# Performance work log

Hardware: AMD Instinct MI355X
Metric: run time of the kernel (lower is better)

## Reference

```python
import jax, jax.numpy as jnp
import numpy as np

B, D, T, R = 8, 128, 32768, 2
C = D // R  # reduced channel dim = 64


def conv1x1(x, w, b):
    # x: [B, Cin, T], w: [Cout, Cin], b: [Cout] -> [B, Cout, T]
    return jnp.einsum('oi,bit->bot', w, x) + b[None, :, None]


def setup_inputs() -> dict:
    key = jax.random.key(0)
    ks = jax.random.split(key, 16)
    inp = {
        'x1': jax.random.normal(ks[0], (B, D, T), dtype=jnp.float32),
        'x2': jnp.zeros((B, D, T), dtype=jnp.float32),  # unused in encoder stage
        'mask': jnp.ones((B, 1, T), dtype=jnp.float32),
        # 1x1 conv projections (weights squeezed to [out, in])
        'wq': jax.random.normal(ks[1], (C, D), dtype=jnp.float32) * 0.05,
        'bq': jnp.zeros((C,), dtype=jnp.float32),
        'wk': jax.random.normal(ks[2], (C, D), dtype=jnp.float32) * 0.05,
        'bk': jnp.zeros((C,), dtype=jnp.float32),
        'wv': jax.random.normal(ks[3], (C, D), dtype=jnp.float32) * 0.05,
        'bv': jnp.zeros((C,), dtype=jnp.float32),
        # E, F: Linear(C -> C) with bias
        'we': jax.random.normal(ks[4], (C, C), dtype=jnp.float32) * 0.1,
        'be': jnp.zeros((C,), dtype=jnp.float32),
        'wf': jax.random.normal(ks[5], (C, C), dtype=jnp.float32) * 0.1,
        'bf': jnp.zeros((C,), dtype=jnp.float32),
        # output 1x1 conv: C -> D
        'wo': jax.random.normal(ks[6], (D, C), dtype=jnp.float32) * 0.05,
        'bo': jnp.zeros((D,), dtype=jnp.float32),
    }
    return inp


def reference(x1, x2, mask, wq, bq, wk, bk, wv, bv, we, be, wf, bf, wo, bo):
    # Q/K/V projections (encoder stage: value from x1; x2 unused)
    Q = conv1x1(x1, wq, bq)              # [B, C, T]
    K = conv1x1(x1, wk, bk)              # [B, C, T]
    V = conv1x1(x1, wv, bv)              # [B, C, T]
    # K = E(K^T): [B, T, C] @ we^T + be
    Kp = jnp.einsum('bct,oc->bto', K, we) + be  # [B, T, C]
    # S = Q @ Kp -> [B, C, C], scaled by sqrt(last dim)
    S = jnp.einsum('bct,btk->bck', Q, Kp)
    P = jax.nn.softmax(S / jnp.sqrt(jnp.asarray(S.shape[-1], S.dtype)), axis=-1)
    # dropout is identity in eval mode
    # V = (F(V^T))^T: [B, C, T]
    Vp = jnp.einsum('bct,oc->bot', V, wf) + bf[None, :, None]  # [B, C, T]
    out = jnp.einsum('bck,bkt->bct', P, Vp)  # [B, C, T]
    out = conv1x1(jax.nn.relu(out), wo, bo)  # [B, D, T]
    return out * mask[:, 0:1, :]
```

## Files before the change

### kernel.cpp

```cpp
#include <hip/hip_runtime.h>
#include <stdint.h>
#include <stddef.h>

#define B_ 8
#define D_ 128
#define T_ 32768
#define C_ 64
#define NCH_ 128

typedef __bf16 bf16;
typedef __bf16 bf16x4 __attribute__((ext_vector_type(4)));
typedef __bf16 bf16x8 __attribute__((ext_vector_type(8)));
typedef float f32x4 __attribute__((ext_vector_type(4)));
typedef float f32x16 __attribute__((ext_vector_type(16)));

__device__ __forceinline__ f32x16 zero16() {
  f32x16 z;
#pragma unroll
  for (int i = 0; i < 16; ++i) z[i] = 0.f;
  return z;
}

__global__ __launch_bounds__(256) void k0_zero(float* __restrict__ p, int n)
{
  int i = blockIdx.x * 256 + threadIdx.x;
  if (i < n) p[i] = 0.f;
}

__global__ __launch_bounds__(256, 4) void k1_gram(
    const float* __restrict__ x1,
    const float* __restrict__ we, const float* __restrict__ wk,
    const float* __restrict__ bk, const float* __restrict__ be,
    const float* __restrict__ wf, const float* __restrict__ wv,
    const float* __restrict__ bv, const float* __restrict__ bfv,
    const float* __restrict__ wo,
    float* __restrict__ G, float* __restrict__ r,
    float* __restrict__ wkp, float* __restrict__ wvp,
    float* __restrict__ bkp, float* __restrict__ bvp,
    bf16* __restrict__ wobf,
    float* __restrict__ gpart)
{
  const int blk = blockIdx.x;
  const int tid = threadIdx.x;
  const int ngram = B_ * NCH_;

  if (blk >= ngram) {
    const int wb = blk - ngram;
    if (wb < 64) {
      const float* wa  = (wb < 32) ? we : wf;
      const float* wb2 = (wb < 32) ? wk : wv;
      float* outw      = (wb < 32) ? wkp : wvp;
      const int idx = (wb & 31) * 256 + tid;
      const int o = idx >> 7, d = idx & 127;
      float s = 0.f;
      for (int c = 0; c < 64; ++c) s += wa[o * 64 + c] * wb2[c * 128 + d];
      outw[idx] = s;
      if (tid < 64) {
        if (wb == 0) {
          float t = 0.f;
          for (int c = 0; c < 64; ++c) t += we[tid * 64 + c] * bk[c];
          bkp[tid] = t + be[tid];
        } else if (wb == 32) {
          float t = 0.f;
          for (int c = 0; c < 64; ++c) t += wf[tid * 64 + c] * bv[c];
          bvp[tid] = t + bfv[tid];
        }
      }
    } else {
      const int idx = (wb - 64) * 256 + tid;
      wobf[idx] = (bf16)wo[idx];
    }
    return;
  }

  __shared__ bf16 x_s[128 * 72];

  const int b  = blk >> 7;
  const int ch = blk & (NCH_ - 1);
  const int t0 = ch * (T_ / NCH_);
  const int wave = tid >> 6, lane = tid & 63;
  const int lrow = lane & 31, lk = lane >> 5;
  const int qa = wave >> 1, qb = wave & 1;

  const float* xb = x1 + (size_t)b * D_ * T_;

  f32x16 acc00 = zero16(), acc01 = zero16(), acc10 = zero16(), acc11 = zero16();
  float rsum = 0.f;

  const int scol = (tid & 15) * 4;
  const int srow0 = tid >> 4;

  const bf16* A0  = &x_s[(64 * qa + lrow) * 72 + 8 * lk];
  const bf16* A1  = A0 + 32 * 72;
  const bf16* Bb0 = &x_s[(64 * qb + lrow) * 72 + 8 * lk];
  const bf16* Bb1 = Bb0 + 32 * 72;

  f32x4 pre[8];
#pragma unroll
  for (int it = 0; it < 8; ++it) {
    const int row = it * 16 + srow0;
    pre[it] = *(const f32x4*)(xb + (size_t)row * T_ + t0 + scol);
  }

  for (int s = 0; s < 4; ++s) {
    if (s) __syncthreads();
#pragma unroll
    for (int it = 0; it < 8; ++it) {
      const int row = it * 16 + srow0;
      bf16x4 h;
#pragma unroll
      for (int j = 0; j < 4; ++j) h[j] = (bf16)pre[it][j];
      *(bf16x4*)&x_s[row * 72 + scol] = h;
    }
    __syncthreads();
    if (s < 3) {
      const int tb = t0 + (s + 1) * 64;
#pragma unroll
      for (int it = 0; it < 8; ++it) {
        const int row = it * 16 + srow0;
        pre[it] = *(const f32x4*)(xb + (size_t)row * T_ + tb + scol);
      }
    }
#pragma unroll
    for (int k = 0; k < 4; ++k) {
      bf16x8 fa0 = *(const bf16x8*)(A0 + 16 * k);
      bf16x8 fa1 = *(const bf16x8*)(A1 + 16 * k);
      bf16x8 fb0 = *(const bf16x8*)(Bb0 + 16 * k);
      bf16x8 fb1 = *(const bf16x8*)(Bb1 + 16 * k);
      bf16x8 own = qb ? fa1 : fa0;
#pragma unroll
      for (int j = 0; j < 8; ++j) rsum += (float)own[j];
      acc00 = __builtin_amdgcn_mfma_f32_32x32x16_bf16(fa0, fb0, acc00, 0, 0, 0);
      acc01 = __builtin_amdgcn_mfma_f32_32x32x16_bf16(fa0, fb1, acc01, 0, 0, 0);
      acc10 = __builtin_amdgcn_mfma_f32_32x32x16_bf16(fa1, fb0, acc10, 0, 0, 0);
      acc11 = __builtin_amdgcn_mfma_f32_32x32x16_bf16(fa1, fb1, acc11, 0, 0, 0);
    }
  }

  if (gpart) {
    float* gp = gpart + (size_t)blk * 16384;
#pragma unroll
    for (int rr = 0; rr < 16; ++rr) {
      const int rloc = (rr & 3) + 8 * (rr >> 2) + 4 * lk;
      const int r0 = 64 * qa + rloc, r1 = 64 * qa + 32 + rloc;
      const int c0 = 64 * qb + lrow, c1 = 64 * qb + 32 + lrow;
      gp[r0 * 128 + c0] = acc00[rr];
      gp[r0 * 128 + c1] = acc01[rr];
      gp[r1 * 128 + c0] = acc10[rr];
      gp[r1 * 128 + c1] = acc11[rr];
    }
  } else {
    float* gb = G + (size_t)b * 16384;
#pragma unroll
    for (int rr = 0; rr < 16; ++rr) {
      const int rloc = (rr & 3) + 8 * (rr >> 2) + 4 * lk;
      const int r0 = 64 * qa + rloc, r1 = 64 * qa + 32 + rloc;
      const int c0 = 64 * qb + lrow, c1 = 64 * qb + 32 + lrow;
      atomicAdd(&gb[r0 * 128 + c0], acc00[rr]);
      atomicAdd(&gb[r0 * 128 + c1], acc01[rr]);
      atomicAdd(&gb[r1 * 128 + c0], acc10[rr]);
      atomicAdd(&gb[r1 * 128 + c1], acc11[rr]);
    }
  }
  float rtot = rsum + __shfl_xor(rsum, 32, 64);
  if (lk == 0) atomicAdd(&r[b * 128 + 32 * wave + lrow], rtot);
}

__global__ __launch_bounds__(256) void k2_reduce(
    const float* __restrict__ gpart, float* __restrict__ G)
{
  const int g4 = blockIdx.x * 256 + threadIdx.x;
  const int b = g4 >> 12;
  const int e4 = g4 & 4095;
  const f32x4* p = (const f32x4*)(gpart + ((size_t)b * NCH_) * 16384) + e4;
  f32x4 s = {0.f, 0.f, 0.f, 0.f};
#pragma unroll 8
  for (int ch = 0; ch < NCH_; ++ch) s += p[(size_t)ch * 4096];
  *((f32x4*)G + g4) = s;
}

__global__ __launch_bounds__(128) void k3_softmax(
    const float* __restrict__ wq, const float* __restrict__ bq,
    const float* __restrict__ G, const float* __restrict__ r,
    const float* __restrict__ wkp, const float* __restrict__ wvp,
    const float* __restrict__ bkp, const float* __restrict__ bvp,
    bf16* __restrict__ attw, float* __restrict__ attb)
{
  const int b = blockIdx.x >> 6, c = blockIdx.x & 63;
  const int tid = threadIdx.x;
  __shared__ float sM[128], sR[128], sQ[128], sP[64];
  __shared__ float sRed;

  const float* Gb = G + (size_t)b * 16384;
  const float* wqc = wq + c * 128;

  const float rv = r[b * 128 + tid];
  sR[tid] = rv;
  float m = 0.f;
  for (int j = 0; j < 128; ++j) m += wqc[j] * Gb[j * 128 + tid];
  sM[tid] = m;
  sQ[tid] = wqc[tid] * rv;
  __syncthreads();

  if (tid < 64) {
    float q2 = sQ[tid] + sQ[tid + 64];
#pragma unroll
    for (int off = 32; off; off >>= 1) q2 += __shfl_xor(q2, off, 64);
    if (tid == 0) sRed = q2;
  }
  __syncthreads();
  const float qr = sRed;
  const float bqc = bq[c];

  if (tid < 64) {
    const int k = tid;
    float s = 0.f, wkr = 0.f;
    for (int i = 0; i < 128; ++i) {
      const float w = wkp[k * 128 + i];
      s += sM[i] * w;
      wkr += sR[i] * w;
    }
    const float bk2 = bkp[k];
    float logit = (s + bqc * wkr + bk2 * qr + (float)T_ * bqc * bk2) * 0.125f;
    float mx = logit;
#pragma unroll
    for (int off = 32; off; off >>= 1) mx = fmaxf(mx, __shfl_xor(mx, off, 64));
    const float e = __expf(logit - mx);
    float sum = e;
#pragma unroll
    for (int off = 32; off; off >>= 1) sum += __shfl_xor(sum, off, 64);
    sP[k] = e / sum;
  }
  __syncthreads();

  {
    float aw = 0.f;
    for (int k = 0; k < 64; ++k) aw += sP[k] * wvp[k * 128 + tid];
    attw[((size_t)b * 64 + c) * 128 + tid] = (bf16)aw;
  }
  if (tid < 64) {
    float pb = sP[tid] * bvp[tid];
#pragma unroll
    for (int off = 32; off; off >>= 1) pb += __shfl_xor(pb, off, 64);
    if (tid == 0) attb[b * 64 + c] = pb;
  }
}

__global__ __launch_bounds__(256, 4) void k4_out(
    const float* __restrict__ x1, const float* __restrict__ mask,
    const bf16* __restrict__ wobf, const float* __restrict__ bo,
    const bf16* __restrict__ attw, const float* __restrict__ attb,
    float* __restrict__ out)
{
  __shared__ bf16 m1[128 * 72];
  __shared__ float bo_s[128];
  __shared__ float ab_s[64];

  const int b = blockIdx.x >> 8;
  const int t0 = (blockIdx.x & 255) << 7;
  const int tid = threadIdx.x;
  const int wave = tid >> 6, lane = tid & 63;
  const int lrow = lane & 31, lk = lane >> 5;
  const int tcol = 32 * wave + lrow;

  if (tid < 128) bo_s[tid] = bo[tid];
  if (tid < 64) ab_s[tid] = attb[b * 64 + tid];
  __syncthreads();

  const float* xc = x1 + (size_t)b * D_ * T_ + t0 + tcol;
  const bf16* awb = attw + (size_t)b * 8192;

  f32x16 p0 = zero16(), p1 = zero16();
#pragma unroll
  for (int k0 = 0; k0 < 8; ++k0) {
    bf16x8 a0 = *(const bf16x8*)(awb + (size_t)lrow * 128 + 16 * k0 + 8 * lk);
    bf16x8 a1 = *(const bf16x8*)(awb + (size_t)(32 + lrow) * 128 + 16 * k0 + 8 * lk);
    bf16x8 bx;
#pragma unroll
    for (int j = 0; j < 8; ++j)
      bx[j] = (bf16)xc[(size_t)(16 * k0 + 8 * lk + j) * T_];
    p0 = __builtin_amdgcn_mfma_f32_32x32x16_bf16(a0, bx, p0, 0, 0, 0);
    p1 = __builtin_amdgcn_mfma_f32_32x32x16_bf16(a1, bx, p1, 0, 0, 0);
  }
  bf16* mrow = &m1[tcol * 72];
#pragma unroll
  for (int rr = 0; rr < 16; ++rr) {
    const int row = (rr & 3) + 8 * (rr >> 2) + 4 * lk;
    mrow[row]      = (bf16)fmaxf(p0[rr] + ab_s[row], 0.f);
    mrow[32 + row] = (bf16)fmaxf(p1[rr] + ab_s[32 + row], 0.f);
  }

  f32x16 q0 = zero16(), q1 = zero16(), q2 = zero16(), q3 = zero16();
#pragma unroll
  for (int k0 = 0; k0 < 4; ++k0) {
    bf16x8 bm = *(const bf16x8*)(mrow + 16 * k0 + 8 * lk);
    bf16x8 w0 = *(const bf16x8*)(wobf + (size_t)(lrow) * 64 + 16 * k0 + 8 * lk);
    bf16x8 w1 = *(const bf16x8*)(wobf + (size_t)(32 + lrow) * 64 + 16 * k0 + 8 * lk);
    bf16x8 w2 = *(const bf16x8*)(wobf + (size_t)(64 + lrow) * 64 + 16 * k0 + 8 * lk);
    bf16x8 w3 = *(const bf16x8*)(wobf + (size_t)(96 + lrow) * 64 + 16 * k0 + 8 * lk);
    q0 = __builtin_amdgcn_mfma_f32_32x32x16_bf16(w0, bm, q0, 0, 0, 0);
    q1 = __builtin_amdgcn_mfma_f32_32x32x16_bf16(w1, bm, q1, 0, 0, 0);
    q2 = __builtin_amdgcn_mfma_f32_32x32x16_bf16(w2, bm, q2, 0, 0, 0);
    q3 = __builtin_amdgcn_mfma_f32_32x32x16_bf16(w3, bm, q3, 0, 0, 0);
  }

  const float mv = mask[(size_t)b * T_ + t0 + tcol];
  float* ob = out + (size_t)b * D_ * T_ + t0 + tcol;
#pragma unroll
  for (int rr = 0; rr < 16; ++rr) {
    const int row = (rr & 3) + 8 * (rr >> 2) + 4 * lk;
    ob[(size_t)(row) * T_]      = (q0[rr] + bo_s[row]) * mv;
    ob[(size_t)(32 + row) * T_] = (q1[rr] + bo_s[32 + row]) * mv;
    ob[(size_t)(64 + row) * T_] = (q2[rr] + bo_s[64 + row]) * mv;
    ob[(size_t)(96 + row) * T_] = (q3[rr] + bo_s[96 + row]) * mv;
  }
}

extern "C" void kernel_launch(void* const* d_in, const int* in_sizes, int n_in,
                              void* d_out, int out_size, void* d_ws, size_t ws_size,
                              hipStream_t stream)
{
  const float* x1   = (const float*)d_in[0];
  const float* mask = (const float*)d_in[2];
  const float* wq   = (const float*)d_in[3];
  const float* bq   = (const float*)d_in[4];
  const float* wk   = (const float*)d_in[5];
  const float* bk   = (const float*)d_in[6];
  const float* wv   = (const float*)d_in[7];
  const float* bv   = (const float*)d_in[8];
  const float* we   = (const float*)d_in[9];
  const float* be   = (const float*)d_in[10];
  const float* wf   = (const float*)d_in[11];
  const float* bfv  = (const float*)d_in[12];
  const float* wo   = (const float*)d_in[13];
  const float* bo   = (const float*)d_in[14];
  float* out = (float*)d_out;

  char* base = (char*)d_ws;
  size_t off = 0;
  float* G    = (float*)(base + off); off += (size_t)B_ * 16384 * 4;
  float* r    = (float*)(base + off); off += (size_t)B_ * 128 * 4;
  float* wkp  = (float*)(base + off); off += 8192 * 4;
  float* wvp  = (float*)(base + off); off += 8192 * 4;
  float* bkp  = (float*)(base + off); off += 64 * 4;
  float* bvp  = (float*)(base + off); off += 64 * 4;
  float* attb = (float*)(base + off); off += (size_t)B_ * 64 * 4;
  bf16* attw  = (bf16*)(base + off);  off += (size_t)B_ * 64 * 128 * 2;
  bf16* wobf  = (bf16*)(base + off);  off += 8192 * 2;
  off = (off + 15) & ~(size_t)15;
  float* gpart = (float*)(base + off);
  const size_t need = off + (size_t)B_ * NCH_ * 16384 * 4;
  const bool use_part = (ws_size >= need);
  if (!use_part) gpart = nullptr;

  if (use_part) {
    k0_zero<<<(B_ * 128 + 255) / 256, 256, 0, stream>>>(r, B_ * 128);
  } else {
    const int nzero = B_ * 16384 + B_ * 128;
    k0_zero<<<(nzero + 255) / 256, 256, 0, stream>>>(G, nzero);
  }
  k1_gram<<<B_ * NCH_ + 96, 256, 0, stream>>>(
      x1, we, wk, bk, be, wf, wv, bv, bfv, wo,
      G, r, wkp, wvp, bkp, bvp, wobf, gpart);
  if (use_part)
    k2_reduce<<<(B_ * 16384) / (256 * 4), 256, 0, stream>>>(gpart, G);
  k3_softmax<<<B_ * 64, 128, 0, stream>>>(wq, bq, G, r, wkp, wvp, bkp, bvp, attw, attb);
  k4_out<<<B_ * (T_ / 128), 256, 0, stream>>>(x1, mask, wobf, bo, attw, attb, out);
}
```

Before: 435.6 us.

## Stage x and output through LDS for coalesced loads and stores in gram and output kernels

The gram kernel now loads the whole 256-column chunk into LDS in one pass instead of four double-buffered 64-column stages. Partial gram tiles are written as contiguous per-wave vectors, and the reduce kernel scatters them into the final layout. The output kernel replaces strided per-element x loads with coalesced row loads transposed into LDS. It also stages results through LDS so global stores become row-contiguous. Occupancy hints drop from 4 to 2 blocks to accommodate the larger shared memory, which costs latency hiding.

```diff
diff --git a/kernel.cpp b/kernel.cpp
--- a/kernel.cpp
+++ b/kernel.cpp
@@ -11,6 +11,7 @@
 typedef __bf16 bf16;
 typedef __bf16 bf16x4 __attribute__((ext_vector_type(4)));
 typedef __bf16 bf16x8 __attribute__((ext_vector_type(8)));
+typedef float f32x2 __attribute__((ext_vector_type(2)));
 typedef float f32x4 __attribute__((ext_vector_type(4)));
 typedef float f32x16 __attribute__((ext_vector_type(16)));
 
@@ -27,7 +28,7 @@
   if (i < n) p[i] = 0.f;
 }
 
-__global__ __launch_bounds__(256, 4) void k1_gram(
+__global__ __launch_bounds__(256, 2) void k1_gram(
     const float* __restrict__ x1,
     const float* __restrict__ we, const float* __restrict__ wk,
     const float* __restrict__ bk, const float* __restrict__ be,
@@ -73,7 +74,7 @@
     return;
   }
 
-  __shared__ bf16 x_s[128 * 72];
+  __shared__ bf16 x_s[128 * 264];
 
   const int b  = blk >> 7;
   const int ch = blk & (NCH_ - 1);
@@ -82,72 +83,57 @@
   const int lrow = lane & 31, lk = lane >> 5;
   const int qa = wave >> 1, qb = wave & 1;
 
-  const float* xb = x1 + (size_t)b * D_ * T_;
+  const float* xb = x1 + (size_t)b * D_ * T_ + t0;
+
+#pragma unroll
+  for (int g = 0; g < 4; ++g) {
+    f32x4 pre[8];
+#pragma unroll
+    for (int i = 0; i < 8; ++i) {
+      const int row = 32 * wave + 8 * g + i;
+      pre[i] = *(const f32x4*)(xb + (size_t)row * T_ + 4 * lane);
+    }
+#pragma unroll
+    for (int i = 0; i < 8; ++i) {
+      const int row = 32 * wave + 8 * g + i;
+      bf16x4 h;
+#pragma unroll
+      for (int j = 0; j < 4; ++j) h[j] = (bf16)pre[i][j];
+      *(bf16x4*)&x_s[row * 264 + 4 * lane] = h;
+    }
+  }
+  __syncthreads();
 
   f32x16 acc00 = zero16(), acc01 = zero16(), acc10 = zero16(), acc11 = zero16();
   float rsum = 0.f;
 
-  const int scol = (tid & 15) * 4;
-  const int srow0 = tid >> 4;
-
-  const bf16* A0  = &x_s[(64 * qa + lrow) * 72 + 8 * lk];
-  const bf16* A1  = A0 + 32 * 72;
-  const bf16* Bb0 = &x_s[(64 * qb + lrow) * 72 + 8 * lk];
-  const bf16* Bb1 = Bb0 + 32 * 72;
-
-  f32x4 pre[8];
-#pragma unroll
-  for (int it = 0; it < 8; ++it) {
-    const int row = it * 16 + srow0;
-    pre[it] = *(const f32x4*)(xb + (size_t)row * T_ + t0 + scol);
-  }
-
-  for (int s = 0; s < 4; ++s) {
-    if (s) __syncthreads();
-#pragma unroll
-    for (int it = 0; it < 8; ++it) {
-      const int row = it * 16 + srow0;
-      bf16x4 h;
-#pragma unroll
-      for (int j = 0; j < 4; ++j) h[j] = (bf16)pre[it][j];
-      *(bf16x4*)&x_s[row * 72 + scol] = h;
-    }
-    __syncthreads();
-    if (s < 3) {
-      const int tb = t0 + (s + 1) * 64;
-#pragma unroll
-      for (int it = 0; it < 8; ++it) {
-        const int row = it * 16 + srow0;
-        pre[it] = *(const f32x4*)(xb + (size_t)row * T_ + tb + scol);
-      }
-    }
-#pragma unroll
-    for (int k = 0; k < 4; ++k) {
-      bf16x8 fa0 = *(const bf16x8*)(A0 + 16 * k);
-      bf16x8 fa1 = *(const bf16x8*)(A1 + 16 * k);
-      bf16x8 fb0 = *(const bf16x8*)(Bb0 + 16 * k);
-      bf16x8 fb1 = *(const bf16x8*)(Bb1 + 16 * k);
-      bf16x8 own = qb ? fa1 : fa0;
-#pragma unroll
-      for (int j = 0; j < 8; ++j) rsum += (float)own[j];
-      acc00 = __builtin_amdgcn_mfma_f32_32x32x16_bf16(fa0, fb0, acc00, 0, 0, 0);
-      acc01 = __builtin_amdgcn_mfma_f32_32x32x16_bf16(fa0, fb1, acc01, 0, 0, 0);
-      acc10 = __builtin_amdgcn_mfma_f32_32x32x16_bf16(fa1, fb0, acc10, 0, 0, 0);
-      acc11 = __builtin_amdgcn_mfma_f32_32x32x16_bf16(fa1, fb1, acc11, 0, 0, 0);
-    }
+  const bf16* A0  = &x_s[(64 * qa + lrow) * 264 + 8 * lk];
+  const bf16* A1  = A0 + 32 * 264;
+  const bf16* Bb0 = &x_s[(64 * qb + lrow) * 264 + 8 * lk];
+  const bf16* Bb1 = Bb0 + 32 * 264;
+
+#pragma unroll
+  for (int k = 0; k < 16; ++k) {
+    bf16x8 fa0 = *(const bf16x8*)(A0 + 16 * k);
+    bf16x8 fa1 = *(const bf16x8*)(A1 + 16 * k);
+    bf16x8 fb0 = *(const bf16x8*)(Bb0 + 16 * k);
+    bf16x8 fb1 = *(const bf16x8*)(Bb1 + 16 * k);
+    bf16x8 own = qb ? fa1 : fa0;
+#pragma unroll
+    for (int j = 0; j < 8; ++j) rsum += (float)own[j];
+    acc00 = __builtin_amdgcn_mfma_f32_32x32x16_bf16(fa0, fb0, acc00, 0, 0, 0);
+    acc01 = __builtin_amdgcn_mfma_f32_32x32x16_bf16(fa0, fb1, acc01, 0, 0, 0);
+    acc10 = __builtin_amdgcn_mfma_f32_32x32x16_bf16(fa1, fb0, acc10, 0, 0, 0);
+    acc11 = __builtin_amdgcn_mfma_f32_32x32x16_bf16(fa1, fb1, acc11, 0, 0, 0);
   }
 
   if (gpart) {
-    float* gp = gpart + (size_t)blk * 16384;
+    float* gp = gpart + (size_t)blk * 16384 + wave * 4096;
 #pragma unroll
     for (int rr = 0; rr < 16; ++rr) {
-      const int rloc = (rr & 3) + 8 * (rr >> 2) + 4 * lk;
-      const int r0 = 64 * qa + rloc, r1 = 64 * qa + 32 + rloc;
-      const int c0 = 64 * qb + lrow, c1 = 64 * qb + 32 + lrow;
-      gp[r0 * 128 + c0] = acc00[rr];
-      gp[r0 * 128 + c1] = acc01[rr];
-      gp[r1 * 128 + c0] = acc10[rr];
-      gp[r1 * 128 + c1] = acc11[rr];
+      f32x4 v;
+      v[0] = acc00[rr]; v[1] = acc01[rr]; v[2] = acc10[rr]; v[3] = acc11[rr];
+      *(f32x4*)(gp + rr * 256 + lane * 4) = v;
     }
   } else {
     float* gb = G + (size_t)b * 16384;
@@ -176,7 +162,17 @@
   f32x4 s = {0.f, 0.f, 0.f, 0.f};
 #pragma unroll 8
   for (int ch = 0; ch < NCH_; ++ch) s += p[(size_t)ch * 4096];
-  *((f32x4*)G + g4) = s;
+
+  const int w = e4 >> 10, rr = (e4 >> 6) & 15, lane = e4 & 63;
+  const int lk = lane >> 5, lrow = lane & 31;
+  const int qa = w >> 1, qb = w & 1;
+  const int rloc = (rr & 3) + 8 * (rr >> 2) + 4 * lk;
+  const int r0 = 64 * qa + rloc, c0 = 64 * qb + lrow;
+  float* Gb = G + (size_t)b * 16384;
+  Gb[r0 * 128 + c0]               = s[0];
+  Gb[r0 * 128 + c0 + 32]          = s[1];
+  Gb[(r0 + 32) * 128 + c0]        = s[2];
+  Gb[(r0 + 32) * 128 + c0 + 32]   = s[3];
 }
 
 __global__ __launch_bounds__(128) void k3_softmax(
@@ -246,13 +242,16 @@
   }
 }
 
-__global__ __launch_bounds__(256, 4) void k4_out(
+__global__ __launch_bounds__(256, 2) void k4_out(
     const float* __restrict__ x1, const float* __restrict__ mask,
     const bf16* __restrict__ wobf, const float* __restrict__ bo,
     const bf16* __restrict__ attw, const float* __restrict__ attb,
     float* __restrict__ out)
 {
-  __shared__ bf16 m1[128 * 72];
+  __shared__ __attribute__((aligned(16))) char buf[128 * 136 * 2];
+  bf16*  x_st = (bf16*)buf;
+  float* o_s  = (float*)buf;
+  __shared__ bf16 m1t[128 * 72];
   __shared__ float bo_s[128];
   __shared__ float ab_s[64];
 
@@ -261,36 +260,49 @@
   const int tid = threadIdx.x;
   const int wave = tid >> 6, lane = tid & 63;
   const int lrow = lane & 31, lk = lane >> 5;
-  const int tcol = 32 * wave + lrow;
 
   if (tid < 128) bo_s[tid] = bo[tid];
   if (tid < 64) ab_s[tid] = attb[b * 64 + tid];
-  __syncthreads();
-
-  const float* xc = x1 + (size_t)b * D_ * T_ + t0 + tcol;
+
+  const float* xb = x1 + (size_t)b * D_ * T_ + t0;
+#pragma unroll
+  for (int g = 0; g < 4; ++g) {
+    f32x2 pr[8];
+#pragma unroll
+    for (int i = 0; i < 8; ++i) {
+      const int d = 32 * wave + 8 * g + i;
+      pr[i] = *(const f32x2*)(xb + (size_t)d * T_ + 2 * lane);
+    }
+#pragma unroll
+    for (int i = 0; i < 8; ++i) {
+      const int d = 32 * wave + 8 * g + i;
+      x_st[(2 * lane) * 136 + d]     = (bf16)pr[i][0];
+      x_st[(2 * lane + 1) * 136 + d] = (bf16)pr[i][1];
+    }
+  }
+  __syncthreads();
+
   const bf16* awb = attw + (size_t)b * 8192;
-
-  f32x16 p0 = zero16(), p1 = zero16();
-#pragma unroll
-  for (int k0 = 0; k0 < 8; ++k0) {
-    bf16x8 a0 = *(const bf16x8*)(awb + (size_t)lrow * 128 + 16 * k0 + 8 * lk);
-    bf16x8 a1 = *(const bf16x8*)(awb + (size_t)(32 + lrow) * 128 + 16 * k0 + 8 * lk);
-    bf16x8 bx;
-#pragma unroll
-    for (int j = 0; j < 8; ++j)
-      bx[j] = (bf16)xc[(size_t)(16 * k0 + 8 * lk + j) * T_];
-    p0 = __builtin_amdgcn_mfma_f32_32x32x16_bf16(a0, bx, p0, 0, 0, 0);
-    p1 = __builtin_amdgcn_mfma_f32_32x32x16_bf16(a1, bx, p1, 0, 0, 0);
-  }
-  bf16* mrow = &m1[tcol * 72];
+  f32x16 m0 = zero16(), m1a = zero16();
+  const bf16* ax = &x_st[(32 * wave + lrow) * 136 + 8 * lk];
+#pragma unroll
+  for (int ki = 0; ki < 8; ++ki) {
+    bf16x8 af = *(const bf16x8*)(ax + 16 * ki);
+    bf16x8 b0 = *(const bf16x8*)(awb + (size_t)lrow * 128 + 16 * ki + 8 * lk);
+    bf16x8 b1 = *(const bf16x8*)(awb + (size_t)(32 + lrow) * 128 + 16 * ki + 8 * lk);
+    m0  = __builtin_amdgcn_mfma_f32_32x32x16_bf16(af, b0, m0, 0, 0, 0);
+    m1a = __builtin_amdgcn_mfma_f32_32x32x16_bf16(af, b1, m1a, 0, 0, 0);
+  }
 #pragma unroll
   for (int rr = 0; rr < 16; ++rr) {
-    const int row = (rr & 3) + 8 * (rr >> 2) + 4 * lk;
-    mrow[row]      = (bf16)fmaxf(p0[rr] + ab_s[row], 0.f);
-    mrow[32 + row] = (bf16)fmaxf(p1[rr] + ab_s[32 + row], 0.f);
-  }
+    const int tl = 32 * wave + (rr & 3) + 8 * (rr >> 2) + 4 * lk;
+    m1t[tl * 72 + lrow]      = (bf16)fmaxf(m0[rr]  + ab_s[lrow], 0.f);
+    m1t[tl * 72 + 32 + lrow] = (bf16)fmaxf(m1a[rr] + ab_s[32 + lrow], 0.f);
+  }
+  __syncthreads();
 
   f32x16 q0 = zero16(), q1 = zero16(), q2 = zero16(), q3 = zero16();
+  const bf16* mrow = &m1t[(32 * wave + lrow) * 72];
 #pragma unroll
   for (int k0 = 0; k0 < 4; ++k0) {
     bf16x8 bm = *(const bf16x8*)(mrow + 16 * k0 + 8 * lk);
@@ -304,15 +316,37 @@
     q3 = __builtin_amdgcn_mfma_f32_32x32x16_bf16(w3, bm, q3, 0, 0, 0);
   }
 
-  const float mv = mask[(size_t)b * T_ + t0 + tcol];
-  float* ob = out + (size_t)b * D_ * T_ + t0 + tcol;
+  const int tl = 32 * wave + lrow;
+  const float mv = mask[(size_t)b * T_ + t0 + tl];
+  float* ob = out + (size_t)b * D_ * T_ + t0;
+
 #pragma unroll
   for (int rr = 0; rr < 16; ++rr) {
-    const int row = (rr & 3) + 8 * (rr >> 2) + 4 * lk;
-    ob[(size_t)(row) * T_]      = (q0[rr] + bo_s[row]) * mv;
-    ob[(size_t)(32 + row) * T_] = (q1[rr] + bo_s[32 + row]) * mv;
-    ob[(size_t)(64 + row) * T_] = (q2[rr] + bo_s[64 + row]) * mv;
-    ob[(size_t)(96 + row) * T_] = (q3[rr] + bo_s[96 + row]) * mv;
+    const int rloc = (rr & 3) + 8 * (rr >> 2) + 4 * lk;
+    o_s[rloc * 132 + tl]        = (q0[rr] + bo_s[rloc]) * mv;
+    o_s[(32 + rloc) * 132 + tl] = (q1[rr] + bo_s[32 + rloc]) * mv;
+  }
+  __syncthreads();
+#pragma unroll
+  for (int i = 0; i < 16; ++i) {
+    const int dl = 16 * wave + i;
+    f32x2 v = *(const f32x2*)(o_s + dl * 132 + 2 * lane);
+    *(f32x2*)(ob + (size_t)dl * T_ + 2 * lane) = v;
+  }
+  __syncthreads();
+
+#pragma unroll
+  for (int rr = 0; rr < 16; ++rr) {
+    const int rloc = (rr & 3) + 8 * (rr >> 2) + 4 * lk;
+    o_s[rloc * 132 + tl]        = (q2[rr] + bo_s[64 + rloc]) * mv;
+    o_s[(32 + rloc) * 132 + tl] = (q3[rr] + bo_s[96 + rloc]) * mv;
+  }
+  __syncthreads();
+#pragma unroll
+  for (int i = 0; i < 16; ++i) {
+    const int dl = 16 * wave + i;
+    f32x2 v = *(const f32x2*)(o_s + dl * 132 + 2 * lane);
+    *(f32x2*)(ob + (size_t)(64 + dl) * T_ + 2 * lane) = v;
   }
 }
 
```

Measured after the change: 394.9 us. 9.3% less time.
